# Optimization experiments

Hardware: AMD Instinct MI355X
Metric: run time of the kernel (lower is better)

Reference implementation:

```python
import jax, jax.numpy as jnp
import numpy as np

N = 50000      # nodes
E = 800000     # edges (before self loops)
IN = 128       # in_channels
HID = 128      # 2*out_channels
OUT = 64       # out_channels
NEG_SLOPE = 0.2


def _gat_conv(x, src, dst, W, a_src, a_dst, b, n_nodes):
    """Single-head PyG GATConv (concat=True, heads=1, self-loops already added)."""
    h = x @ W                                   # [N, F]
    alpha_s = h @ a_src                         # [N]
    alpha_d = h @ a_dst                         # [N]
    e = alpha_s[src] + alpha_d[dst]             # [E'] logits per edge j->i
    e = jnp.where(e > 0, e, NEG_SLOPE * e)      # LeakyReLU(0.2)
    # segment softmax over destination node
    m = jax.ops.segment_max(e, dst, num_segments=n_nodes)   # [N]
    w = jnp.exp(e - m[dst])                                   # [E']
    denom = jax.ops.segment_sum(w, dst, num_segments=n_nodes) # [N]
    alpha = w / denom[dst]                                     # [E']
    out = jax.ops.segment_sum(alpha[:, None] * h[src], dst, num_segments=n_nodes)
    return out + b


def _with_self_loops(edge_index, n_nodes):
    loop = jnp.arange(n_nodes, dtype=edge_index.dtype)
    src = jnp.concatenate([edge_index[0], loop])
    dst = jnp.concatenate([edge_index[1], loop])
    return src, dst


def setup_inputs() -> dict:
    key = jax.random.key(0)
    ks = jax.random.split(key, 10)
    s = 0.1
    return {
        "x": jax.random.normal(ks[0], (N, IN), jnp.float32),
        "edge_index": jax.random.randint(ks[1], (2, E), 0, N, jnp.int32),
        "W1": jax.random.normal(ks[2], (IN, HID), jnp.float32) * s,
        "a1_src": jax.random.normal(ks[3], (HID,), jnp.float32) * s,
        "a1_dst": jax.random.normal(ks[4], (HID,), jnp.float32) * s,
        "b1": jnp.zeros((HID,), jnp.float32),
        "W2": jax.random.normal(ks[5], (HID, OUT), jnp.float32) * s,
        "a2_src": jax.random.normal(ks[6], (OUT,), jnp.float32) * s,
        "a2_dst": jax.random.normal(ks[7], (OUT,), jnp.float32) * s,
        "b2": jnp.zeros((OUT,), jnp.float32),
    }


def reference(x, edge_index, W1, a1_src, a1_dst, b1, W2, a2_src, a2_dst, b2):
    src, dst = _with_self_loops(edge_index, N)
    h = _gat_conv(x, src, dst, W1, a1_src, a1_dst, b1, N)
    h = jax.nn.relu(h)
    return _gat_conv(h, src, dst, W2, a2_src, a2_dst, b2, N)
```

## Files before the change

kernel.cpp:

```cpp
#include <hip/hip_runtime.h>
#include <hip/hip_bf16.h>


#define BCAP 4096

typedef __attribute__((ext_vector_type(8))) short bf16x8;
typedef __attribute__((ext_vector_type(4))) float f32x4;

__device__ __forceinline__ unsigned short bf16bits(float f){
  __hip_bfloat16 b = __float2bfloat16(f);
  return *(unsigned short*)&b;
}
__device__ __forceinline__ float bf16lo(unsigned int v){ return __uint_as_float(v << 16); }
__device__ __forceinline__ float bf16hi(unsigned int v){ return __uint_as_float(v & 0xFFFF0000u); }

__global__ __launch_bounds__(256) void prep_all(
    const float* __restrict__ W1, const float* __restrict__ W2,
    const float* __restrict__ a2s, const float* __restrict__ a2d,
    unsigned short* __restrict__ W1t, unsigned short* __restrict__ W2t,
    float* __restrict__ vas, float* __restrict__ vad,
    int* __restrict__ bucketCount)
{
  int b = blockIdx.x, t = threadIdx.x;
  if (b < 48){
    int idx = b*256 + t;
    if (idx < 8192){
      int n = idx >> 6, k2 = idx & 63;
      float a = W1[(size_t)(2*k2)*128 + n];
      float c = W1[(size_t)(2*k2+1)*128 + n];
      ushort2 o; o.x = bf16bits(a); o.y = bf16bits(c);
      *(ushort2*)&W1t[(size_t)n*128 + 2*k2] = o;
    } else {
      int r = idx - 8192;
      int n = r >> 6, k2 = r & 63;
      float a = W2[(size_t)(2*k2)*64 + n];
      float c = W2[(size_t)(2*k2+1)*64 + n];
      ushort2 o; o.x = bf16bits(a); o.y = bf16bits(c);
      *(ushort2*)&W2t[(size_t)n*128 + 2*k2] = o;
    }
  } else if (b == 48){
    int k = t & 127;
    const float* av = (t < 128) ? a2s : a2d;
    float* ov = (t < 128) ? vas : vad;
    float s = 0.f;
    for (int n=0; n<64; n++) s += W2[(size_t)k*64 + n] * av[n];
    ov[k] = s;
  } else {
    bucketCount[t] = 0; bucketCount[t+256] = 0;
  }
}

template<int NC, bool FUSE>
__device__ __forceinline__ void gemm_body(
    const float* __restrict__ Af, const unsigned short* __restrict__ Ah,
    const unsigned short* __restrict__ Wt,
    const float* __restrict__ avs, const float* __restrict__ avd,
    unsigned short* __restrict__ H, float* __restrict__ as_, float* __restrict__ ad_,
    int M, int rowBase, unsigned short* As, unsigned short* Ws)
{
  const int K = 128;
  int t = threadIdx.x;
  if (Af){
    #pragma unroll
    for (int i=0;i<8;i++){
      int idx = t + i*256; int r = idx>>5, k4 = idx&31;
      int grow = rowBase + r;
      float4 v = (grow<M) ? *(const float4*)&Af[(size_t)grow*K + k4*4]
                          : make_float4(0.f,0.f,0.f,0.f);
      ushort4 o; o.x=bf16bits(v.x); o.y=bf16bits(v.y); o.z=bf16bits(v.z); o.w=bf16bits(v.w);
      *(ushort4*)&As[r*136 + k4*4] = o;
    }
  } else {
    #pragma unroll
    for (int i=0;i<4;i++){
      int idx = t + i*256; int r = idx>>4, k8 = idx&15;
      int grow = rowBase + r;
      uint4 v = (grow<M) ? *(const uint4*)&Ah[(size_t)grow*K + k8*8]
                         : make_uint4(0u,0u,0u,0u);
      *(uint4*)&As[r*136 + k8*8] = v;
    }
  }
  int wave = t>>6, lane = t&63, ln = lane&15, q = lane>>4;
  f32x4 acc[NC/16];
  #pragma unroll
  for (int nt=0; nt<NC/16; nt++) acc[nt] = (f32x4){0.f,0.f,0.f,0.f};

  #pragma unroll
  for (int ch=0; ch<NC/64; ++ch){
    __syncthreads();
    #pragma unroll
    for (int i=0;i<4;i++){
      int idx = t + i*256; int n = idx>>4, k8 = idx&15;
      *(uint4*)&Ws[n*136 + k8*8] = *(const uint4*)&Wt[(size_t)(ch*64+n)*K + k8*8];
    }
    __syncthreads();
    #pragma unroll
    for (int kk=0;kk<4;kk++){
      bf16x8 a = *(const bf16x8*)&As[(wave*16+ln)*136 + kk*32 + q*8];
      #pragma unroll
      for (int nt=0; nt<4; nt++){
        bf16x8 b = *(const bf16x8*)&Ws[(nt*16+ln)*136 + kk*32 + q*8];
        acc[ch*4+nt] = __builtin_amdgcn_mfma_f32_16x16x32_bf16(a, b, acc[ch*4+nt], 0, 0, 0);
      }
    }
  }
  float asl[NC/16], adl[NC/16];
  if (FUSE){
    #pragma unroll
    for (int nt=0; nt<NC/16; nt++){ asl[nt]=avs[nt*16+ln]; adl[nt]=avd[nt*16+ln]; }
  }
  #pragma unroll
  for (int i=0;i<4;i++){
    int grow = rowBase + wave*16 + q*4 + i;
    if (grow < M){
      float ps=0.f, pd=0.f;
      #pragma unroll
      for (int nt=0; nt<NC/16; nt++){
        float v = acc[nt][i];
        H[(size_t)grow*NC + nt*16 + ln] = bf16bits(v);
        if (FUSE){ ps += v*asl[nt]; pd += v*adl[nt]; }
      }
      if (FUSE){
        #pragma unroll
        for (int d=1; d<16; d<<=1){ ps += __shfl_xor(ps,d); pd += __shfl_xor(pd,d); }
        if (ln==0){ as_[grow] = ps; ad_[grow] = pd; }
      }
    }
  }
}

__global__ __launch_bounds__(256) void scatter_or_gemm(
    const int* __restrict__ src, const int* __restrict__ dst,
    int* __restrict__ bucketCount, unsigned int* __restrict__ gbuf, int E, int SB,
    const float* __restrict__ x, const unsigned short* __restrict__ W1t,
    const float* __restrict__ a1s, const float* __restrict__ a1d,
    unsigned short* __restrict__ h1, float* __restrict__ as1, float* __restrict__ ad1,
    int M)
{
  __shared__ unsigned short smem[64*136 + 64*136];
  int t = threadIdx.x;
  if ((int)blockIdx.x >= SB){
    gemm_body<128, true>(x, nullptr, W1t, a1s, a1d, h1, as1, ad1, M,
                         (blockIdx.x - SB)*64, smem, smem + 64*136);
    return;
  }
  int* hist = (int*)smem;
  int* base = hist + 512;
  int e0 = blockIdx.x * 4096;
  hist[t] = 0; hist[t+256] = 0;
  __syncthreads();
  int sv[16], dv[16];
  #pragma unroll
  for (int k=0;k<16;k++){
    int i = e0 + t + k*256;
    if (i < E){ sv[k]=src[i]; dv[k]=dst[i]; atomicAdd(&hist[dv[k]>>7], 1); }
    else { sv[k] = -1; dv[k] = 0; }
  }
  __syncthreads();
  int h0 = hist[t], h1c = hist[t+256];
  if (h0 > 0)  base[t]     = atomicAdd(&bucketCount[t],     h0);
  if (h1c > 0) base[t+256] = atomicAdd(&bucketCount[t+256], h1c);
  __syncthreads();
  hist[t] = 0; hist[t+256] = 0;
  __syncthreads();
  #pragma unroll
  for (int k=0;k<16;k++){
    if (sv[k] >= 0){
      int b = dv[k] >> 7;
      int r = base[b] + atomicAdd(&hist[b], 1);
      if (r < BCAP)
        gbuf[(size_t)b*BCAP + r] = ((unsigned)(dv[k] & 127) << 16) | (unsigned)sv[k];
    }
  }
}

__global__ __launch_bounds__(512) void fine_sort(
    const unsigned int* __restrict__ gbuf, const int* __restrict__ bucketCount,
    int* __restrict__ offs, int* __restrict__ srcS, int N, int E, int B)
{
  __shared__ int sh[512];
  __shared__ int h[128];
  __shared__ int pre[128];
  __shared__ int rank[128];
  int b = blockIdx.x, t = threadIdx.x;
  {
    int nd_t = 0;
    if (t < B){ int lo=t*128; nd_t = (N-lo<128)?(N-lo):128; }
    sh[t] = (t < B ? bucketCount[t] : 0) + nd_t;
    __syncthreads();
    for (int d=1; d<512; d<<=1){
      int x = (t >= d) ? sh[t-d] : 0;
      __syncthreads();
      sh[t] += x;
      __syncthreads();
    }
  }
  int cnt = bucketCount[b]; if (cnt > BCAP) cnt = BCAP;
  int lo = b*128;
  int nd = (N - lo < 128) ? (N - lo) : 128;
  int base = sh[b] - (cnt + nd);
  if (b == 0 && t == 0) offs[N] = E + N;
  if (t < 128){ h[t] = 0; rank[t] = 0; }
  __syncthreads();
  for (int i = t; i < cnt; i += 512)
    atomicAdd(&h[(gbuf[(size_t)b*BCAP + i] >> 16) & 127], 1);
  __syncthreads();
  if (t < 128) pre[t] = (t < nd) ? (h[t] + 1) : 0;
  __syncthreads();
  for (int d=1; d<128; d<<=1){
    int x = (t >= d && t < 128) ? pre[t-d] : 0;
    __syncthreads();
    if (t < 128) pre[t] += x;
    __syncthreads();
  }
  int seg = (t < nd) ? (h[t] + 1) : 0;
  int ex  = (t < 128) ? (pre[t] - seg) : 0;
  if (t < nd){
    offs[lo + t] = base + ex;
    srcS[base + ex] = lo + t;
  }
  __syncthreads();
  if (t < 128) pre[t] = ex;
  __syncthreads();
  for (int i = t; i < cnt; i += 512){
    unsigned e = gbuf[(size_t)b*BCAP + i];
    int dl = (e >> 16) & 127;
    int s  = e & 0xFFFF;
    int r  = atomicAdd(&rank[dl], 1);
    srcS[base + pre[dl] + 1 + r] = s;
  }
}

__global__ __launch_bounds__(256) void edge_agg128(
    const int* __restrict__ offs, const int* __restrict__ srcS,
    const float* __restrict__ asrc, const float* __restrict__ adst,
    const unsigned short* __restrict__ Hin, const float* __restrict__ bias,
    unsigned short* __restrict__ outp,
    const float* __restrict__ vas, const float* __restrict__ vad,
    float* __restrict__ as2, float* __restrict__ ad2, int n)
{
  int wid  = (blockIdx.x * 256 + threadIdx.x) >> 6;
  int lane = threadIdx.x & 63;
  if (wid >= n) return;
  int beg = offs[wid], end = offs[wid+1];
  float ad = adst[wid];
  int qw = lane >> 4, ql = lane & 15;
  float acc[8] = {}; float denom = 0.f;
  for (int base = beg; base < end; base += 64){
    int m = end - base; if (m > 64) m = 64;
    int   sv = (lane < m) ? srcS[base + lane] : 0;
    float av = (lane < m) ? asrc[sv] : 0.f;
    float ev = av + ad;
    ev = (ev > 0.f) ? ev : 0.2f*ev;
    float wv = (lane < m) ? __expf(ev) : 0.f;
    for (int j = 0; j < m; j += 16){
      int i0 = j+qw, i1 = j+4+qw, i2 = j+8+qw, i3 = j+12+qw;
      int   s0 = __shfl(sv,i0), s1 = __shfl(sv,i1), s2 = __shfl(sv,i2), s3 = __shfl(sv,i3);
      float w0 = __shfl(wv,i0), w1 = __shfl(wv,i1), w2 = __shfl(wv,i2), w3 = __shfl(wv,i3);
      uint4 ha = *(const uint4*)&Hin[(size_t)s0*128 + ql*8];
      uint4 hb = *(const uint4*)&Hin[(size_t)s1*128 + ql*8];
      uint4 hc = *(const uint4*)&Hin[(size_t)s2*128 + ql*8];
      uint4 hd = *(const uint4*)&Hin[(size_t)s3*128 + ql*8];
      denom += (w0 + w1) + (w2 + w3);
      acc[0]+=w0*bf16lo(ha.x)+w1*bf16lo(hb.x)+w2*bf16lo(hc.x)+w3*bf16lo(hd.x);
      acc[1]+=w0*bf16hi(ha.x)+w1*bf16hi(hb.x)+w2*bf16hi(hc.x)+w3*bf16hi(hd.x);
      acc[2]+=w0*bf16lo(ha.y)+w1*bf16lo(hb.y)+w2*bf16lo(hc.y)+w3*bf16lo(hd.y);
      acc[3]+=w0*bf16hi(ha.y)+w1*bf16hi(hb.y)+w2*bf16hi(hc.y)+w3*bf16hi(hd.y);
      acc[4]+=w0*bf16lo(ha.z)+w1*bf16lo(hb.z)+w2*bf16lo(hc.z)+w3*bf16lo(hd.z);
      acc[5]+=w0*bf16hi(ha.z)+w1*bf16hi(hb.z)+w2*bf16hi(hc.z)+w3*bf16hi(hd.z);
      acc[6]+=w0*bf16lo(ha.w)+w1*bf16lo(hb.w)+w2*bf16lo(hc.w)+w3*bf16lo(hd.w);
      acc[7]+=w0*bf16hi(ha.w)+w1*bf16hi(hb.w)+w2*bf16hi(hc.w)+w3*bf16hi(hd.w);
    }
  }
  denom += __shfl_xor(denom,16); denom += __shfl_xor(denom,32);
  #pragma unroll
  for (int k=0;k<8;k++){ acc[k]+=__shfl_xor(acc[k],16); acc[k]+=__shfl_xor(acc[k],32); }
  if (qw == 0){
    float inv = 1.0f / denom;
    float ps = 0.f, pd = 0.f;
    unsigned short o[8];
    #pragma unroll
    for (int k=0;k<8;k++){
      float v = fmaxf(acc[k]*inv + bias[ql*8+k], 0.f);
      o[k] = bf16bits(v);
      ps += v * vas[ql*8+k];
      pd += v * vad[ql*8+k];
    }
    *(uint4*)&outp[(size_t)wid*128 + ql*8] = *(uint4*)o;
    #pragma unroll
    for (int d=1; d<16; d<<=1){ ps += __shfl_xor(ps,d); pd += __shfl_xor(pd,d); }
    if (ql == 0){ as2[wid] = ps; ad2[wid] = pd; }
  }
}

__global__ __launch_bounds__(256) void gemm2_k(
    const unsigned short* __restrict__ A, const unsigned short* __restrict__ Wt,
    unsigned short* __restrict__ H, int M)
{
  __shared__ unsigned short smem[64*136 + 64*136];
  gemm_body<64, false>(nullptr, A, Wt, nullptr, nullptr, H, nullptr, nullptr,
                       M, blockIdx.x*64, smem, smem + 64*136);
}

__global__ __launch_bounds__(256) void edge_agg64(
    const int* __restrict__ offs, const int* __restrict__ srcS,
    const float* __restrict__ asrc, const float* __restrict__ adst,
    const unsigned short* __restrict__ Hin, const float* __restrict__ bias,
    float* __restrict__ outp, int n)
{
  int wid  = (blockIdx.x * 256 + threadIdx.x) >> 6;
  int lane = threadIdx.x & 63;
  if (wid >= n) return;
  int beg = offs[wid], end = offs[wid+1];
  float ad = adst[wid];
  int ew = lane >> 3, el = lane & 7;
  float acc[8] = {}; float denom = 0.f;
  for (int base = beg; base < end; base += 64){
    int m = end - base; if (m > 64) m = 64;
    int   sv = (lane < m) ? srcS[base + lane] : 0;
    float av = (lane < m) ? asrc[sv] : 0.f;
    float ev = av + ad;
    ev = (ev > 0.f) ? ev : 0.2f*ev;
    float wv = (lane < m) ? __expf(ev) : 0.f;
    for (int j = 0; j < m; j += 32){
      int i0 = j+ew, i1 = j+8+ew, i2 = j+16+ew, i3 = j+24+ew;
      int   s0 = __shfl(sv,i0), s1 = __shfl(sv,i1), s2 = __shfl(sv,i2), s3 = __shfl(sv,i3);
      float w0 = __shfl(wv,i0), w1 = __shfl(wv,i1), w2 = __shfl(wv,i2), w3 = __shfl(wv,i3);
      uint4 ha = *(const uint4*)&Hin[(size_t)s0*64 + el*8];
      uint4 hb = *(const uint4*)&Hin[(size_t)s1*64 + el*8];
      uint4 hc = *(const uint4*)&Hin[(size_t)s2*64 + el*8];
      uint4 hd = *(const uint4*)&Hin[(size_t)s3*64 + el*8];
      denom += (w0 + w1) + (w2 + w3);
      acc[0]+=w0*bf16lo(ha.x)+w1*bf16lo(hb.x)+w2*bf16lo(hc.x)+w3*bf16lo(hd.x);
      acc[1]+=w0*bf16hi(ha.x)+w1*bf16hi(hb.x)+w2*bf16hi(hc.x)+w3*bf16hi(hd.x);
      acc[2]+=w0*bf16lo(ha.y)+w1*bf16lo(hb.y)+w2*bf16lo(hc.y)+w3*bf16lo(hd.y);
      acc[3]+=w0*bf16hi(ha.y)+w1*bf16hi(hb.y)+w2*bf16hi(hc.y)+w3*bf16hi(hd.y);
      acc[4]+=w0*bf16lo(ha.z)+w1*bf16lo(hb.z)+w2*bf16lo(hc.z)+w3*bf16lo(hd.z);
      acc[5]+=w0*bf16hi(ha.z)+w1*bf16hi(hb.z)+w2*bf16hi(hc.z)+w3*bf16hi(hd.z);
      acc[6]+=w0*bf16lo(ha.w)+w1*bf16lo(hb.w)+w2*bf16lo(hc.w)+w3*bf16lo(hd.w);
      acc[7]+=w0*bf16hi(ha.w)+w1*bf16hi(hb.w)+w2*bf16hi(hc.w)+w3*bf16hi(hd.w);
    }
  }
  denom += __shfl_xor(denom,8); denom += __shfl_xor(denom,16); denom += __shfl_xor(denom,32);
  #pragma unroll
  for (int k=0;k<8;k++){
    acc[k]+=__shfl_xor(acc[k],8); acc[k]+=__shfl_xor(acc[k],16); acc[k]+=__shfl_xor(acc[k],32);
  }
  if (ew == 0){
    float inv = 1.0f / denom;
    float4 o0, o1;
    o0.x = acc[0]*inv + bias[el*8+0]; o0.y = acc[1]*inv + bias[el*8+1];
    o0.z = acc[2]*inv + bias[el*8+2]; o0.w = acc[3]*inv + bias[el*8+3];
    o1.x = acc[4]*inv + bias[el*8+4]; o1.y = acc[5]*inv + bias[el*8+5];
    o1.z = acc[6]*inv + bias[el*8+6]; o1.w = acc[7]*inv + bias[el*8+7];
    *(float4*)&outp[(size_t)wid*64 + el*8]     = o0;
    *(float4*)&outp[(size_t)wid*64 + el*8 + 4] = o1;
  }
}

extern "C" void kernel_launch(void* const* d_in, const int* in_sizes, int n_in,
                              void* d_out, int out_size, void* d_ws, size_t ws_size,
                              hipStream_t stream) {
  const int IN = 128, HID = 128, OUT = 64;
  const int N = in_sizes[0] / IN;
  const int E = in_sizes[1] / 2;
  const int B = (N + 127) / 128;
  const int SB = (E + 4095) / 4096;

  const float* x    = (const float*)d_in[0];
  const int*   ei   = (const int*)d_in[1];
  const float* W1   = (const float*)d_in[2];
  const float* a1s  = (const float*)d_in[3];
  const float* a1d  = (const float*)d_in[4];
  const float* b1   = (const float*)d_in[5];
  const float* W2   = (const float*)d_in[6];
  const float* a2s  = (const float*)d_in[7];
  const float* a2d  = (const float*)d_in[8];
  const float* b2   = (const float*)d_in[9];
  float* out = (float*)d_out;

  char* w = (char*)d_ws;
  unsigned short* W1t = (unsigned short*)w; w += (size_t)HID*IN*2;
  unsigned short* W2t = (unsigned short*)w; w += (size_t)OUT*HID*2;
  unsigned short* h1    = (unsigned short*)w; w += (size_t)N*128*2;
  unsigned short* hrelu = (unsigned short*)w; w += (size_t)N*128*2;
  unsigned short* h2 = h1;
  float* as1   = (float*)w; w += (size_t)N*4;
  float* ad1   = (float*)w; w += (size_t)N*4;
  float* as2   = (float*)w; w += (size_t)N*4;
  float* ad2   = (float*)w; w += (size_t)N*4;
  float* vas   = (float*)w; w += 128*4;
  float* vad   = (float*)w; w += 128*4;
  int* offs    = (int*)w;   w += (size_t)(N+1)*4;
  int* bucketCount = (int*)w; w += 512*4;
  int* srcS    = (int*)w;   w += (size_t)(E+N)*4;
  unsigned int* gbuf = (unsigned int*)w; w += (size_t)B*BCAP*4;

  const int* esrc = ei;
  const int* edst = ei + E;

  hipLaunchKernelGGL(prep_all, dim3(50), dim3(256), 0, stream,
                     W1, W2, a2s, a2d, W1t, W2t, vas, vad, bucketCount);
  hipLaunchKernelGGL(scatter_or_gemm, dim3(SB + (N+63)/64), dim3(256), 0, stream,
                     esrc, edst, bucketCount, gbuf, E, SB,
                     x, W1t, a1s, a1d, h1, as1, ad1, N);
  hipLaunchKernelGGL(fine_sort, dim3(B), dim3(512), 0, stream,
                     gbuf, bucketCount, offs, srcS, N, E, B);
  hipLaunchKernelGGL(edge_agg128, dim3((N*64+255)/256), dim3(256), 0, stream,
                     offs, srcS, as1, ad1, h1, b1, hrelu, vas, vad, as2, ad2, N);
  hipLaunchKernelGGL(gemm2_k, dim3((N+63)/64), dim3(256), 0, stream,
                     hrelu, W2t, h2, N);
  hipLaunchKernelGGL(edge_agg64, dim3((N*64+255)/256), dim3(256), 0, stream,
                     offs, srcS, as2, ad2, h2, b2, out, N);
}
```

Measured before the change: 186.6 us.

## Precompute per-edge attention weights and map one node per wave subgroup

Edge exp weights for layer 1 are now computed inside fine_sort and stored in CSR order, along with a per-edge destination array. Layer-2 weights are computed by extra blocks added to the gemm2 launch. The aggregation kernels now give each node a 16-lane (layer 1) or 8-lane (layer 2) subgroup instead of a full 64-lane wave, which removes the cross-group shuffle reductions and the idle lanes on low-degree nodes. The cost is extra global traffic for the weight and destination arrays, and divergence when nodes sharing a wave have different degrees.

```diff
diff --git a/kernel.cpp b/kernel.cpp
--- a/kernel.cpp
+++ b/kernel.cpp
@@ -13,6 +13,10 @@
 }
 __device__ __forceinline__ float bf16lo(unsigned int v){ return __uint_as_float(v << 16); }
 __device__ __forceinline__ float bf16hi(unsigned int v){ return __uint_as_float(v & 0xFFFF0000u); }
+__device__ __forceinline__ float leaky_exp(float e){
+  e = (e > 0.f) ? e : 0.2f*e;
+  return __expf(e);
+}
 
 __global__ __launch_bounds__(256) void prep_all(
     const float* __restrict__ W1, const float* __restrict__ W2,
@@ -176,7 +180,10 @@
 
 __global__ __launch_bounds__(512) void fine_sort(
     const unsigned int* __restrict__ gbuf, const int* __restrict__ bucketCount,
-    int* __restrict__ offs, int* __restrict__ srcS, int N, int E, int B)
+    int* __restrict__ offs, int* __restrict__ srcS,
+    const float* __restrict__ as1, const float* __restrict__ ad1,
+    float* __restrict__ wS1, unsigned short* __restrict__ dstS,
+    int N, int E, int B)
 {
   __shared__ int sh[512];
   __shared__ int h[128];
@@ -216,8 +223,11 @@
   int seg = (t < nd) ? (h[t] + 1) : 0;
   int ex  = (t < 128) ? (pre[t] - seg) : 0;
   if (t < nd){
-    offs[lo + t] = base + ex;
-    srcS[base + ex] = lo + t;
+    int v = lo + t;
+    offs[v] = base + ex;
+    srcS[base + ex] = v;
+    wS1[base + ex]  = leaky_exp(as1[v] + ad1[v]);
+    dstS[base + ex] = (unsigned short)v;
   }
   __syncthreads();
   if (t < 128) pre[t] = ex;
@@ -227,13 +237,16 @@
     int dl = (e >> 16) & 127;
     int s  = e & 0xFFFF;
     int r  = atomicAdd(&rank[dl], 1);
-    srcS[base + pre[dl] + 1 + r] = s;
+    int pos = base + pre[dl] + 1 + r;
+    srcS[pos] = s;
+    wS1[pos]  = leaky_exp(as1[s] + ad1[lo + dl]);
+    dstS[pos] = (unsigned short)(lo + dl);
   }
 }
 
 __global__ __launch_bounds__(256) void edge_agg128(
     const int* __restrict__ offs, const int* __restrict__ srcS,
-    const float* __restrict__ asrc, const float* __restrict__ adst,
+    const float* __restrict__ wS,
     const unsigned short* __restrict__ Hin, const float* __restrict__ bias,
     unsigned short* __restrict__ outp,
     const float* __restrict__ vas, const float* __restrict__ vad,
@@ -241,27 +254,27 @@
 {
   int wid  = (blockIdx.x * 256 + threadIdx.x) >> 6;
   int lane = threadIdx.x & 63;
-  if (wid >= n) return;
-  int beg = offs[wid], end = offs[wid+1];
-  float ad = adst[wid];
   int qw = lane >> 4, ql = lane & 15;
-  float acc[8] = {}; float denom = 0.f;
-  for (int base = beg; base < end; base += 64){
-    int m = end - base; if (m > 64) m = 64;
-    int   sv = (lane < m) ? srcS[base + lane] : 0;
-    float av = (lane < m) ? asrc[sv] : 0.f;
-    float ev = av + ad;
-    ev = (ev > 0.f) ? ev : 0.2f*ev;
-    float wv = (lane < m) ? __expf(ev) : 0.f;
-    for (int j = 0; j < m; j += 16){
-      int i0 = j+qw, i1 = j+4+qw, i2 = j+8+qw, i3 = j+12+qw;
-      int   s0 = __shfl(sv,i0), s1 = __shfl(sv,i1), s2 = __shfl(sv,i2), s3 = __shfl(sv,i3);
-      float w0 = __shfl(wv,i0), w1 = __shfl(wv,i1), w2 = __shfl(wv,i2), w3 = __shfl(wv,i3);
+  int v = wid*4 + qw;
+  bool alive = (v < n);
+  int beg = 0, end = 0;
+  if (alive){ beg = offs[v]; end = offs[v+1]; }
+  float acc[8] = {}; float dn = 0.f;
+  for (int base = beg; base < end; base += 16){
+    int m = end - base; if (m > 16) m = 16;
+    int sv = 0; float wv = 0.f;
+    if (ql < m){ sv = srcS[base + ql]; wv = wS[base + ql]; }
+    for (int j = 0; j < m; j += 4){
+      int l0 = (qw<<4) + j;
+      int   s0 = __shfl(sv,l0),   s1 = __shfl(sv,l0+1);
+      int   s2 = __shfl(sv,l0+2), s3 = __shfl(sv,l0+3);
+      float w0 = __shfl(wv,l0),   w1 = __shfl(wv,l0+1);
+      float w2 = __shfl(wv,l0+2), w3 = __shfl(wv,l0+3);
       uint4 ha = *(const uint4*)&Hin[(size_t)s0*128 + ql*8];
       uint4 hb = *(const uint4*)&Hin[(size_t)s1*128 + ql*8];
       uint4 hc = *(const uint4*)&Hin[(size_t)s2*128 + ql*8];
       uint4 hd = *(const uint4*)&Hin[(size_t)s3*128 + ql*8];
-      denom += (w0 + w1) + (w2 + w3);
+      dn += (w0 + w1) + (w2 + w3);
       acc[0]+=w0*bf16lo(ha.x)+w1*bf16lo(hb.x)+w2*bf16lo(hc.x)+w3*bf16lo(hd.x);
       acc[1]+=w0*bf16hi(ha.x)+w1*bf16hi(hb.x)+w2*bf16hi(hc.x)+w3*bf16hi(hd.x);
       acc[2]+=w0*bf16lo(ha.y)+w1*bf16lo(hb.y)+w2*bf16lo(hc.y)+w3*bf16lo(hd.y);
@@ -272,65 +285,75 @@
       acc[7]+=w0*bf16hi(ha.w)+w1*bf16hi(hb.w)+w2*bf16hi(hc.w)+w3*bf16hi(hd.w);
     }
   }
-  denom += __shfl_xor(denom,16); denom += __shfl_xor(denom,32);
-  #pragma unroll
-  for (int k=0;k<8;k++){ acc[k]+=__shfl_xor(acc[k],16); acc[k]+=__shfl_xor(acc[k],32); }
-  if (qw == 0){
-    float inv = 1.0f / denom;
+  if (alive){
+    float inv = 1.0f / dn;
     float ps = 0.f, pd = 0.f;
     unsigned short o[8];
     #pragma unroll
     for (int k=0;k<8;k++){
-      float v = fmaxf(acc[k]*inv + bias[ql*8+k], 0.f);
-      o[k] = bf16bits(v);
-      ps += v * vas[ql*8+k];
-      pd += v * vad[ql*8+k];
-    }
-    *(uint4*)&outp[(size_t)wid*128 + ql*8] = *(uint4*)o;
+      float u = fmaxf(acc[k]*inv + bias[ql*8+k], 0.f);
+      o[k] = bf16bits(u);
+      ps += u * vas[ql*8+k];
+      pd += u * vad[ql*8+k];
+    }
+    *(uint4*)&outp[(size_t)v*128 + ql*8] = *(uint4*)o;
     #pragma unroll
     for (int d=1; d<16; d<<=1){ ps += __shfl_xor(ps,d); pd += __shfl_xor(pd,d); }
-    if (ql == 0){ as2[wid] = ps; ad2[wid] = pd; }
-  }
-}
-
-__global__ __launch_bounds__(256) void gemm2_k(
+    if (ql == 0){ as2[v] = ps; ad2[v] = pd; }
+  }
+}
+
+__global__ __launch_bounds__(256) void gemm2_or_wprep(
     const unsigned short* __restrict__ A, const unsigned short* __restrict__ Wt,
-    unsigned short* __restrict__ H, int M)
+    unsigned short* __restrict__ H, int M, int G2B,
+    const int* __restrict__ srcS, const unsigned short* __restrict__ dstS,
+    const float* __restrict__ as2, const float* __restrict__ ad2,
+    float* __restrict__ wS2, int T)
 {
   __shared__ unsigned short smem[64*136 + 64*136];
-  gemm_body<64, false>(nullptr, A, Wt, nullptr, nullptr, H, nullptr, nullptr,
-                       M, blockIdx.x*64, smem, smem + 64*136);
+  if ((int)blockIdx.x < G2B){
+    gemm_body<64, false>(nullptr, A, Wt, nullptr, nullptr, H, nullptr, nullptr,
+                         M, blockIdx.x*64, smem, smem + 64*136);
+    return;
+  }
+  int i0 = (blockIdx.x - G2B)*256 + threadIdx.x;
+  int stride = (gridDim.x - G2B)*256;
+  for (int e = i0; e < T; e += stride){
+    int s = srcS[e];
+    int d = dstS[e];
+    wS2[e] = leaky_exp(as2[s] + ad2[d]);
+  }
 }
 
 __global__ __launch_bounds__(256) void edge_agg64(
     const int* __restrict__ offs, const int* __restrict__ srcS,
-    const float* __restrict__ asrc, const float* __restrict__ adst,
+    const float* __restrict__ wS,
     const unsigned short* __restrict__ Hin, const float* __restrict__ bias,
     float* __restrict__ outp, int n)
 {
   int wid  = (blockIdx.x * 256 + threadIdx.x) >> 6;
   int lane = threadIdx.x & 63;
-  if (wid >= n) return;
-  int beg = offs[wid], end = offs[wid+1];
-  float ad = adst[wid];
   int ew = lane >> 3, el = lane & 7;
-  float acc[8] = {}; float denom = 0.f;
-  for (int base = beg; base < end; base += 64){
-    int m = end - base; if (m > 64) m = 64;
-    int   sv = (lane < m) ? srcS[base + lane] : 0;
-    float av = (lane < m) ? asrc[sv] : 0.f;
-    float ev = av + ad;
-    ev = (ev > 0.f) ? ev : 0.2f*ev;
-    float wv = (lane < m) ? __expf(ev) : 0.f;
-    for (int j = 0; j < m; j += 32){
-      int i0 = j+ew, i1 = j+8+ew, i2 = j+16+ew, i3 = j+24+ew;
-      int   s0 = __shfl(sv,i0), s1 = __shfl(sv,i1), s2 = __shfl(sv,i2), s3 = __shfl(sv,i3);
-      float w0 = __shfl(wv,i0), w1 = __shfl(wv,i1), w2 = __shfl(wv,i2), w3 = __shfl(wv,i3);
+  int v = wid*8 + ew;
+  bool alive = (v < n);
+  int beg = 0, end = 0;
+  if (alive){ beg = offs[v]; end = offs[v+1]; }
+  float acc[8] = {}; float dn = 0.f;
+  for (int base = beg; base < end; base += 8){
+    int m = end - base; if (m > 8) m = 8;
+    int sv = 0; float wv = 0.f;
+    if (el < m){ sv = srcS[base + el]; wv = wS[base + el]; }
+    for (int j = 0; j < m; j += 4){
+      int l0 = (ew<<3) + j;
+      int   s0 = __shfl(sv,l0),   s1 = __shfl(sv,l0+1);
+      int   s2 = __shfl(sv,l0+2), s3 = __shfl(sv,l0+3);
+      float w0 = __shfl(wv,l0),   w1 = __shfl(wv,l0+1);
+      float w2 = __shfl(wv,l0+2), w3 = __shfl(wv,l0+3);
       uint4 ha = *(const uint4*)&Hin[(size_t)s0*64 + el*8];
       uint4 hb = *(const uint4*)&Hin[(size_t)s1*64 + el*8];
       uint4 hc = *(const uint4*)&Hin[(size_t)s2*64 + el*8];
       uint4 hd = *(const uint4*)&Hin[(size_t)s3*64 + el*8];
-      denom += (w0 + w1) + (w2 + w3);
+      dn += (w0 + w1) + (w2 + w3);
       acc[0]+=w0*bf16lo(ha.x)+w1*bf16lo(hb.x)+w2*bf16lo(hc.x)+w3*bf16lo(hd.x);
       acc[1]+=w0*bf16hi(ha.x)+w1*bf16hi(hb.x)+w2*bf16hi(hc.x)+w3*bf16hi(hd.x);
       acc[2]+=w0*bf16lo(ha.y)+w1*bf16lo(hb.y)+w2*bf16lo(hc.y)+w3*bf16lo(hd.y);
@@ -341,20 +364,15 @@
       acc[7]+=w0*bf16hi(ha.w)+w1*bf16hi(hb.w)+w2*bf16hi(hc.w)+w3*bf16hi(hd.w);
     }
   }
-  denom += __shfl_xor(denom,8); denom += __shfl_xor(denom,16); denom += __shfl_xor(denom,32);
-  #pragma unroll
-  for (int k=0;k<8;k++){
-    acc[k]+=__shfl_xor(acc[k],8); acc[k]+=__shfl_xor(acc[k],16); acc[k]+=__shfl_xor(acc[k],32);
-  }
-  if (ew == 0){
-    float inv = 1.0f / denom;
+  if (alive){
+    float inv = 1.0f / dn;
     float4 o0, o1;
     o0.x = acc[0]*inv + bias[el*8+0]; o0.y = acc[1]*inv + bias[el*8+1];
     o0.z = acc[2]*inv + bias[el*8+2]; o0.w = acc[3]*inv + bias[el*8+3];
     o1.x = acc[4]*inv + bias[el*8+4]; o1.y = acc[5]*inv + bias[el*8+5];
     o1.z = acc[6]*inv + bias[el*8+6]; o1.w = acc[7]*inv + bias[el*8+7];
-    *(float4*)&outp[(size_t)wid*64 + el*8]     = o0;
-    *(float4*)&outp[(size_t)wid*64 + el*8 + 4] = o1;
+    *(float4*)&outp[(size_t)v*64 + el*8]     = o0;
+    *(float4*)&outp[(size_t)v*64 + el*8 + 4] = o1;
   }
 }
 
@@ -366,6 +384,7 @@
   const int E = in_sizes[1] / 2;
   const int B = (N + 127) / 128;
   const int SB = (E + 4095) / 4096;
+  const int T = E + N;
 
   const float* x    = (const float*)d_in[0];
   const int*   ei   = (const int*)d_in[1];
@@ -393,7 +412,10 @@
   float* vad   = (float*)w; w += 128*4;
   int* offs    = (int*)w;   w += (size_t)(N+1)*4;
   int* bucketCount = (int*)w; w += 512*4;
-  int* srcS    = (int*)w;   w += (size_t)(E+N)*4;
+  int* srcS    = (int*)w;   w += (size_t)T*4;
+  float* wS1   = (float*)w; w += (size_t)T*4;
+  float* wS2   = (float*)w; w += (size_t)T*4;
+  unsigned short* dstS = (unsigned short*)w; w += ((size_t)T*2 + 3) & ~(size_t)3;
   unsigned int* gbuf = (unsigned int*)w; w += (size_t)B*BCAP*4;
 
   const int* esrc = ei;
@@ -405,11 +427,14 @@
                      esrc, edst, bucketCount, gbuf, E, SB,
                      x, W1t, a1s, a1d, h1, as1, ad1, N);
   hipLaunchKernelGGL(fine_sort, dim3(B), dim3(512), 0, stream,
-                     gbuf, bucketCount, offs, srcS, N, E, B);
-  hipLaunchKernelGGL(edge_agg128, dim3((N*64+255)/256), dim3(256), 0, stream,
-                     offs, srcS, as1, ad1, h1, b1, hrelu, vas, vad, as2, ad2, N);
-  hipLaunchKernelGGL(gemm2_k, dim3((N+63)/64), dim3(256), 0, stream,
-                     hrelu, W2t, h2, N);
-  hipLaunchKernelGGL(edge_agg64, dim3((N*64+255)/256), dim3(256), 0, stream,
-                     offs, srcS, as2, ad2, h2, b2, out, N);
-}
+                     gbuf, bucketCount, offs, srcS, as1, ad1, wS1, dstS, N, E, B);
+  int wv128 = (N + 3) / 4;
+  hipLaunchKernelGGL(edge_agg128, dim3((wv128 + 3) / 4), dim3(256), 0, stream,
+                     offs, srcS, wS1, h1, b1, hrelu, vas, vad, as2, ad2, N);
+  const int G2B = (N + 63) / 64;
+  hipLaunchKernelGGL(gemm2_or_wprep, dim3(G2B + 512), dim3(256), 0, stream,
+                     hrelu, W2t, h2, N, G2B, srcS, dstS, as2, ad2, wS2, T);
+  int wv64 = (N + 7) / 8;
+  hipLaunchKernelGGL(edge_agg64, dim3((wv64 + 3) / 4), dim3(256), 0, stream,
+                     offs, srcS, wS2, h2, b2, out, N);
+}
```

New measurement: 184.1 us. Within noise of the previous version (-1.3%).
